# Performance work log

Hardware: AMD Instinct MI355X
Metric: run time of the kernel (lower is better)

The kernel has to match this reference:

```python
import jax, jax.numpy as jnp
import numpy as np

NUM_HEAD = 8
HEAD_DIM = 64
MAX_LEN = 2048
FEAT_DIM = 512
BATCH = 2
TEMPERATURE = 10000.0


def positional_encoding(L, F, temperature=TEMPERATURE):
    # Faithful port of get_positional_encoding (torch.range is inclusive -> L / F elements)
    embed = jnp.arange(L, dtype=jnp.float32)
    dim_t = jnp.arange(F, dtype=jnp.float32)
    dim_t = temperature ** (2.0 * jnp.floor(dim_t / 2.0) / F)
    pos = embed[:, None] / dim_t                      # (L, F)
    pos = jnp.stack([jnp.sin(pos[:, 0::2]), jnp.cos(pos[:, 1::2])], axis=2)  # (L, F//2, 2)
    return pos.reshape(1, L, F)


def setup_inputs() -> dict:
    key = jax.random.key(0)
    ks = jax.random.split(key, 7)
    D = NUM_HEAD * HEAD_DIM
    scale = 1.0 / np.sqrt(FEAT_DIM)
    return {
        "inputs": jax.random.normal(ks[0], (BATCH, FEAT_DIM, MAX_LEN), dtype=jnp.float32),
        "Wq": jax.random.normal(ks[1], (D, FEAT_DIM), dtype=jnp.float32) * scale,
        "bq": jax.random.normal(ks[2], (D,), dtype=jnp.float32) * 0.01,
        "Wk": jax.random.normal(ks[3], (D, FEAT_DIM), dtype=jnp.float32) * scale,
        "bk": jax.random.normal(ks[4], (D,), dtype=jnp.float32) * 0.01,
        "Wv": jax.random.normal(ks[5], (D, FEAT_DIM), dtype=jnp.float32) * scale,
        "bv": jax.random.normal(ks[6], (D,), dtype=jnp.float32) * 0.01,
    }


def reference(inputs, Wq, bq, Wk, bk, Wv, bv):
    B, F, L = inputs.shape
    H, d = NUM_HEAD, HEAD_DIM
    pos = positional_encoding(L, F)                   # (1, L, F)
    x = jnp.transpose(inputs, (0, 2, 1))              # (B, L, F)
    qk_in = x + pos
    q = (qk_in @ Wq.T + bq).reshape(B, L, H, d)       # (B, L, H, d)
    k = (qk_in @ Wk.T + bk).reshape(B, L, H, d)
    v = x @ Wv.T + bv                                 # computed but unused (bug in original)
    del v
    # NOTE: original uses KEY heads as values (multi_head_value built from key)
    scores = jnp.einsum("bqhd,bkhd->bhqk", q, k) * (float(d) ** -0.5)
    attn = jax.nn.softmax(scores, axis=-1)            # (B, H, L, L)
    dist = jnp.einsum("bhqk,bkhd->bqhd", attn, k).reshape(B, L, H * d)
    attn_out = jnp.transpose(attn, (0, 2, 3, 1))      # (B, L, L, H) == cat of head splits on -1
    return dist, attn_out
```

## Files before the change

kernel.cpp:

```cpp
#include <hip/hip_runtime.h>
#include <math.h>

constexpr int LSEQ = 2048;
constexpr int FEAT = 512;
constexpr int NH = 8;
constexpr int DM = 512;
constexpr int NB = 2;

typedef __bf16 bf16x8 __attribute__((ext_vector_type(8)));
typedef unsigned short u16x8 __attribute__((ext_vector_type(8)));
typedef unsigned int u32x4 __attribute__((ext_vector_type(4)));
typedef float f32x4 __attribute__((ext_vector_type(4)));

__device__ inline f32x4 mfma16(u16x8 a, u16x8 b, f32x4 c) {
  return __builtin_amdgcn_mfma_f32_16x16x32_bf16(
      __builtin_bit_cast(bf16x8, a), __builtin_bit_cast(bf16x8, b), c, 0, 0, 0);
}
__device__ inline unsigned cvtpk(float lo, float hi) {
  unsigned r;
  asm("v_cvt_pk_bf16_f32 %0, %1, %2" : "=v"(r) : "v"(lo), "v"(hi));
  return r;
}
__device__ inline u16x8 ldbf8(const unsigned short* p) {
  return *reinterpret_cast<const u16x8*>(p);
}

__global__ __launch_bounds__(256) void pos_kernel(float* __restrict__ posT) {
  int idx = blockIdx.x * 256 + threadIdx.x;
  int l = idx & (LSEQ - 1);
  int f = idx >> 11;
  int i = f >> 1;
  double t = exp((double)i * (9.210340371976184 / 256.0));
  float ang = (float)((double)l / t);
  posT[idx] = (f & 1) ? cosf(ang) : sinf(ang);
}

__global__ __launch_bounds__(256) void prep_kernel(const float* __restrict__ x,
                                                   const float* __restrict__ posT,
                                                   unsigned short* __restrict__ abuf) {
  __shared__ float As[64 * 68];
  const int t = threadIdx.x;
  const int bid = blockIdx.x;
  const int ft = bid & 7, lt = (bid >> 3) & 31, b = bid >> 8;
  const int f0 = ft * 64, l0 = lt * 64;
#pragma unroll
  for (int rep = 0; rep < 4; ++rep) {
    int fl = rep * 16 + (t >> 4), l4 = (t & 15) * 4;
    float4 xv = *(const float4*)(x + ((size_t)b * FEAT + f0 + fl) * LSEQ + l0 + l4);
    float4 pv = *(const float4*)(posT + (size_t)(f0 + fl) * LSEQ + l0 + l4);
    *(float4*)&As[fl * 68 + l4] = make_float4(xv.x + pv.x, xv.y + pv.y, xv.z + pv.z, xv.w + pv.w);
  }
  __syncthreads();
  const int ll = t >> 2, fc = t & 3;
#pragma unroll
  for (int rep = 0; rep < 4; ++rep) {
    int fb = (fc + rep * 4) * 4;
    float v0 = As[(fb + 0) * 68 + ll];
    float v1 = As[(fb + 1) * 68 + ll];
    float v2 = As[(fb + 2) * 68 + ll];
    float v3 = As[(fb + 3) * 68 + ll];
    uint2 u = make_uint2(cvtpk(v0, v1), cvtpk(v2, v3));
    *(uint2*)(abuf + ((size_t)(b * LSEQ + l0 + ll)) * 512 + f0 + fb) = u;
  }
}

__global__ __launch_bounds__(256) void wcvt_kernel(const float* __restrict__ Wq,
                                                   const float* __restrict__ Wk,
                                                   unsigned short* __restrict__ wbuf) {
  int i8 = blockIdx.x * 256 + threadIdx.x;
  size_t base = (size_t)i8 * 8;
  const float* src = (base < (size_t)512 * 512) ? Wq + base : Wk + (base - (size_t)512 * 512);
  float4 a = *(const float4*)src;
  float4 b4 = *(const float4*)(src + 4);
  *(uint2*)(wbuf + base) = make_uint2(cvtpk(a.x, a.y), cvtpk(a.z, a.w));
  *(uint2*)(wbuf + base + 4) = make_uint2(cvtpk(b4.x, b4.y), cvtpk(b4.z, b4.w));
}

__global__ __launch_bounds__(256) void proj_kernel(
    const unsigned short* __restrict__ abuf, const unsigned short* __restrict__ wbuf,
    const float* __restrict__ bq, const float* __restrict__ bk,
    unsigned short* __restrict__ qb, unsigned short* __restrict__ kb,
    unsigned short* __restrict__ kT) {
  const int t = threadIdx.x;
  const int c0 = blockIdx.x * 64;
  const int r0 = blockIdx.y * 64;
  const int w = t >> 6, l = t & 63;
  const int lr = l & 15, g = l >> 4;
  const int c0w = c0 + (w >> 1) * 32;
  const int r0w = r0 + (w & 1) * 32;
  f32x4 acc[2][2];
#pragma unroll
  for (int i = 0; i < 2; ++i)
#pragma unroll
    for (int j = 0; j < 2; ++j) acc[i][j] = (f32x4){0.f, 0.f, 0.f, 0.f};
  for (int f0 = 0; f0 < FEAT; f0 += 32) {
    u16x8 a0 = ldbf8(wbuf + (size_t)(c0w + lr) * 512 + f0 + g * 8);
    u16x8 a1 = ldbf8(wbuf + (size_t)(c0w + 16 + lr) * 512 + f0 + g * 8);
    u16x8 b0 = ldbf8(abuf + (size_t)(r0w + lr) * 512 + f0 + g * 8);
    u16x8 b1 = ldbf8(abuf + (size_t)(r0w + 16 + lr) * 512 + f0 + g * 8);
    acc[0][0] = mfma16(a0, b0, acc[0][0]);
    acc[0][1] = mfma16(a0, b1, acc[0][1]);
    acc[1][0] = mfma16(a1, b0, acc[1][0]);
    acc[1][1] = mfma16(a1, b1, acc[1][1]);
  }
  const int isK = (c0 >= DM);
  const float* bias = isK ? bk : bq;
  unsigned short* ob = isK ? kb : qb;
  const int cb = c0w & (DM - 1);
#pragma unroll
  for (int ch = 0; ch < 2; ++ch) {
    int c = cb + ch * 16 + g * 4;
    float b0v = bias[c], b1v = bias[c + 1], b2v = bias[c + 2], b3v = bias[c + 3];
#pragma unroll
    for (int rh = 0; rh < 2; ++rh) {
      int r = r0w + rh * 16 + lr;
      f32x4 v = acc[ch][rh];
      uint2 u = make_uint2(cvtpk(v[0] + b0v, v[1] + b1v), cvtpk(v[2] + b2v, v[3] + b3v));
      *(uint2*)(ob + (size_t)r * 512 + c) = u;
      if (isK) {
        int bsel = r >> 11, lq = r & (LSEQ - 1);
        unsigned short* kp = kT + ((size_t)(bsel * 512 + c)) * 2048 + lq;
        kp[0] = (unsigned short)(u.x & 0xffff);
        kp[2048] = (unsigned short)(u.x >> 16);
        kp[2 * 2048] = (unsigned short)(u.y & 0xffff);
        kp[3 * 2048] = (unsigned short)(u.y >> 16);
      }
    }
  }
}

__global__ __launch_bounds__(512) void pass1_kernel(
    const unsigned short* __restrict__ qb, const unsigned short* __restrict__ kb,
    float* __restrict__ lpart) {
  const int t = threadIdx.x;
  const int bid = blockIdx.x;
  const int sp = bid & 3, qt = (bid >> 2) & 63, b = bid >> 8;
  const int q0 = qt * 32;
  const int h = t >> 6, l = t & 63;
  const int lr = l & 15, g = l >> 4;
  u16x8 qf[2][2];
#pragma unroll
  for (int Mt = 0; Mt < 2; ++Mt)
#pragma unroll
    for (int dh = 0; dh < 2; ++dh)
      qf[Mt][dh] = ldbf8(qb + (size_t)(b * LSEQ + q0 + Mt * 16 + lr) * 512 + h * 64 + dh * 32 + g * 8);
  float sum[2] = {0.f, 0.f};
  for (int slab = 0; slab < 16; ++slab) {
    const int kk0 = sp * 512 + slab * 32;
    u16x8 af[2][2];
#pragma unroll
    for (int kh = 0; kh < 2; ++kh)
#pragma unroll
      for (int dh = 0; dh < 2; ++dh)
        af[kh][dh] = ldbf8(kb + (size_t)(b * LSEQ + kk0 + kh * 16 + lr) * 512 + h * 64 + dh * 32 + g * 8);
#pragma unroll
    for (int Mt = 0; Mt < 2; ++Mt)
#pragma unroll
      for (int kh = 0; kh < 2; ++kh) {
        f32x4 s = (f32x4){0.f, 0.f, 0.f, 0.f};
        s = mfma16(af[kh][0], qf[Mt][0], s);
        s = mfma16(af[kh][1], qf[Mt][1], s);
        sum[Mt] += __expf(s[0] * 0.125f) + __expf(s[1] * 0.125f) +
                   __expf(s[2] * 0.125f) + __expf(s[3] * 0.125f);
      }
  }
#pragma unroll
  for (int Mt = 0; Mt < 2; ++Mt) {
    float v = sum[Mt];
    v += __shfl_xor(v, 16);
    v += __shfl_xor(v, 32);
    if ((l & 48) == 0)
      lpart[((size_t)((b * 4 + sp) * LSEQ) + q0 + Mt * 16 + lr) * 8 + h] = v;
  }
}

__global__ __launch_bounds__(512) void pass2_kernel(
    const unsigned short* __restrict__ qb, const unsigned short* __restrict__ kb,
    const unsigned short* __restrict__ kT, const float* __restrict__ lpart,
    float* __restrict__ attn, float* __restrict__ distp, int log2S) {
  __shared__ float Ps[32 * 292];
  __shared__ float linv[256];
  const int t = threadIdx.x;
  const int bid = blockIdx.x;
  const int S = 1 << log2S;
  const int sp = bid & (S - 1);
  const int qt = (bid >> log2S) & 63;
  const int b = bid >> (6 + log2S);
  const int q0 = qt * 32;
  if (t < 256) {
    int q = t >> 3, hh = t & 7;
    float s = 0.f;
#pragma unroll
    for (int p = 0; p < 4; ++p)
      s += lpart[((size_t)((b * 4 + p) * LSEQ) + q0 + q) * 8 + hh];
    linv[t] = 1.0f / s;
  }
  __syncthreads();
  const int h = t >> 6, l = t & 63;
  const int lr = l & 15, g = l >> 4;
  u16x8 qf[2][2];
#pragma unroll
  for (int Mt = 0; Mt < 2; ++Mt)
#pragma unroll
    for (int dh = 0; dh < 2; ++dh)
      qf[Mt][dh] = ldbf8(qb + (size_t)(b * LSEQ + q0 + Mt * 16 + lr) * 512 + h * 64 + dh * 32 + g * 8);
  float lv[2] = {linv[lr * 8 + h], linv[(16 + lr) * 8 + h]};
  f32x4 dacc[2][4];
#pragma unroll
  for (int Mt = 0; Mt < 2; ++Mt)
#pragma unroll
    for (int Nd = 0; Nd < 4; ++Nd) dacc[Mt][Nd] = (f32x4){0.f, 0.f, 0.f, 0.f};

  const int nslab = 64 >> log2S;
  const int kkb = sp * (2048 >> log2S);
  for (int slab = 0; slab < nslab; ++slab) {
    const int kk0 = kkb + slab * 32;
    u16x8 af[2][2];
#pragma unroll
    for (int kh = 0; kh < 2; ++kh)
#pragma unroll
      for (int dh = 0; dh < 2; ++dh)
        af[kh][dh] = ldbf8(kb + (size_t)(b * LSEQ + kk0 + kh * 16 + lr) * 512 + h * 64 + dh * 32 + g * 8);
    u16x8 bt[4];
#pragma unroll
    for (int Nd = 0; Nd < 4; ++Nd)
      bt[Nd] = ldbf8(kT + (size_t)(b * 512 + h * 64 + Nd * 16 + lr) * 2048 + kk0 + g * 8);
#pragma unroll
    for (int Mt = 0; Mt < 2; ++Mt)
#pragma unroll
      for (int kh = 0; kh < 2; ++kh) {
        f32x4 s = (f32x4){0.f, 0.f, 0.f, 0.f};
        s = mfma16(af[kh][0], qf[Mt][0], s);
        s = mfma16(af[kh][1], qf[Mt][1], s);
        float e0 = __expf(s[0] * 0.125f) * lv[Mt];
        float e1 = __expf(s[1] * 0.125f) * lv[Mt];
        float e2 = __expf(s[2] * 0.125f) * lv[Mt];
        float e3 = __expf(s[3] * 0.125f) * lv[Mt];
        int base = (Mt * 16 + lr) * 292 + h * 36 + kh * 16 + g * 4;
        *(float2*)&Ps[base] = make_float2(e0, e1);
        *(float2*)&Ps[base + 2] = make_float2(e2, e3);
      }
    __syncthreads();
#pragma unroll
    for (int rep = 0; rep < 4; ++rep) {
      int F = rep * 512 + t;
      int q = F >> 6, kk = (F >> 1) & 31, hh = (F & 1) * 4;
      int pb = q * 292 + hh * 36 + kk;
      float4 v = make_float4(Ps[pb], Ps[pb + 36], Ps[pb + 72], Ps[pb + 108]);
      *(float4*)(attn + ((size_t)(b * LSEQ + q0 + q)) * (LSEQ * NH) + (size_t)(kk0 + kk) * 8 + hh) = v;
    }
#pragma unroll
    for (int Mt = 0; Mt < 2; ++Mt) {
      int pb = (Mt * 16 + lr) * 292 + h * 36 + g * 8;
      f32x4 plo = *(const f32x4*)&Ps[pb];
      f32x4 phi = *(const f32x4*)&Ps[pb + 4];
      u32x4 pu = {cvtpk(plo[0], plo[1]), cvtpk(plo[2], plo[3]),
                  cvtpk(phi[0], phi[1]), cvtpk(phi[2], phi[3])};
      u16x8 pa = __builtin_bit_cast(u16x8, pu);
#pragma unroll
      for (int Nd = 0; Nd < 4; ++Nd)
        dacc[Mt][Nd] = mfma16(pa, bt[Nd], dacc[Mt][Nd]);
    }
    __syncthreads();
  }
  float* dp = distp + (size_t)sp * (NB * LSEQ * DM);
#pragma unroll
  for (int Mt = 0; Mt < 2; ++Mt)
#pragma unroll
    for (int Nd = 0; Nd < 4; ++Nd)
#pragma unroll
      for (int r = 0; r < 4; ++r)
        dp[((size_t)(b * LSEQ + q0 + Mt * 16 + g * 4 + r)) * 512 + h * 64 + Nd * 16 + lr] =
            dacc[Mt][Nd][r];
}

__global__ __launch_bounds__(256) void combine_kernel(const float* __restrict__ p,
                                                      float* __restrict__ dist) {
  int i4 = blockIdx.x * 256 + threadIdx.x;
  const int N4 = (NB * LSEQ * DM) / 4;
  const float4* p4 = (const float4*)p;
  float4 a = p4[i4], c = p4[N4 + i4];
  ((float4*)dist)[i4] = make_float4(a.x + c.x, a.y + c.y, a.z + c.z, a.w + c.w);
}

extern "C" void kernel_launch(void* const* d_in, const int* in_sizes, int n_in,
                              void* d_out, int out_size, void* d_ws, size_t ws_size,
                              hipStream_t stream) {
  const float* x  = (const float*)d_in[0];
  const float* Wq = (const float*)d_in[1];
  const float* bq = (const float*)d_in[2];
  const float* Wk = (const float*)d_in[3];
  const float* bk = (const float*)d_in[4];
  float* out  = (float*)d_out;
  float* dist = out;
  float* attn = out + (size_t)NB * LSEQ * DM;
  float* ws = (float*)d_ws;
  float* posT  = ws;
  float* lpart = ws + 1048576;
  unsigned short* abuf = (unsigned short*)(ws + 1179648);
  unsigned short* wbuf = (unsigned short*)(ws + 2228224);
  unsigned short* qb   = (unsigned short*)(ws + 2490368);
  unsigned short* kb   = (unsigned short*)(ws + 3538944);
  unsigned short* kT   = (unsigned short*)(ws + 4587520);
  float* distp = ws + 5636096;
  const int log2S = (ws_size >= (size_t)(5636096 + 2ull * 2097152) * 4) ? 1 : 0;

  pos_kernel<<<4096, 256, 0, stream>>>(posT);
  prep_kernel<<<512, 256, 0, stream>>>(x, posT, abuf);
  wcvt_kernel<<<256, 256, 0, stream>>>(Wq, Wk, wbuf);
  proj_kernel<<<dim3(16, 64), 256, 0, stream>>>(abuf, wbuf, bq, bk, qb, kb, kT);
  pass1_kernel<<<512, 512, 0, stream>>>(qb, kb, lpart);
  float* dtarget = (log2S == 0) ? dist : distp;
  pass2_kernel<<<NB * 64 * (1 << log2S), 512, 0, stream>>>(qb, kb, kT, lpart, attn, dtarget, log2S);
  if (log2S)
    combine_kernel<<<2048, 256, 0, stream>>>(distp, dist);
}
```

Baseline: 178.9 us.

## Split pass2 into four key partitions, use exp2, nontemporal attn stores

Allows pass2 to split the key range four ways when the workspace is large enough, raising the block count to fill more CUs, and generalizes the combine kernel to sum S partials. Replaces __expf of the scaled score with exp2f and a pre-multiplied log2e constant. Writes the large attention output with nontemporal stores to avoid cache pollution, and adds a min-blocks hint to launch bounds. In exchange, the extra split costs more partial-sum memory traffic in combine, and the occupancy hint may force register spills.

```diff
diff --git a/kernel.cpp b/kernel.cpp
--- a/kernel.cpp
+++ b/kernel.cpp
@@ -11,6 +11,8 @@
 typedef unsigned short u16x8 __attribute__((ext_vector_type(8)));
 typedef unsigned int u32x4 __attribute__((ext_vector_type(4)));
 typedef float f32x4 __attribute__((ext_vector_type(4)));
+
+#define EXPC 0.18033688011112042f
 
 __device__ inline f32x4 mfma16(u16x8 a, u16x8 b, f32x4 c) {
   return __builtin_amdgcn_mfma_f32_16x16x32_bf16(
@@ -129,7 +131,7 @@
   }
 }
 
-__global__ __launch_bounds__(512) void pass1_kernel(
+__global__ __launch_bounds__(512, 4) void pass1_kernel(
     const unsigned short* __restrict__ qb, const unsigned short* __restrict__ kb,
     float* __restrict__ lpart) {
   const int t = threadIdx.x;
@@ -160,8 +162,8 @@
         f32x4 s = (f32x4){0.f, 0.f, 0.f, 0.f};
         s = mfma16(af[kh][0], qf[Mt][0], s);
         s = mfma16(af[kh][1], qf[Mt][1], s);
-        sum[Mt] += __expf(s[0] * 0.125f) + __expf(s[1] * 0.125f) +
-                   __expf(s[2] * 0.125f) + __expf(s[3] * 0.125f);
+        sum[Mt] += exp2f(s[0] * EXPC) + exp2f(s[1] * EXPC) +
+                   exp2f(s[2] * EXPC) + exp2f(s[3] * EXPC);
       }
   }
 #pragma unroll
@@ -174,7 +176,7 @@
   }
 }
 
-__global__ __launch_bounds__(512) void pass2_kernel(
+__global__ __launch_bounds__(512, 4) void pass2_kernel(
     const unsigned short* __restrict__ qb, const unsigned short* __restrict__ kb,
     const unsigned short* __restrict__ kT, const float* __restrict__ lpart,
     float* __restrict__ attn, float* __restrict__ distp, int log2S) {
@@ -232,10 +234,10 @@
         f32x4 s = (f32x4){0.f, 0.f, 0.f, 0.f};
         s = mfma16(af[kh][0], qf[Mt][0], s);
         s = mfma16(af[kh][1], qf[Mt][1], s);
-        float e0 = __expf(s[0] * 0.125f) * lv[Mt];
-        float e1 = __expf(s[1] * 0.125f) * lv[Mt];
-        float e2 = __expf(s[2] * 0.125f) * lv[Mt];
-        float e3 = __expf(s[3] * 0.125f) * lv[Mt];
+        float e0 = exp2f(s[0] * EXPC) * lv[Mt];
+        float e1 = exp2f(s[1] * EXPC) * lv[Mt];
+        float e2 = exp2f(s[2] * EXPC) * lv[Mt];
+        float e3 = exp2f(s[3] * EXPC) * lv[Mt];
         int base = (Mt * 16 + lr) * 292 + h * 36 + kh * 16 + g * 4;
         *(float2*)&Ps[base] = make_float2(e0, e1);
         *(float2*)&Ps[base + 2] = make_float2(e2, e3);
@@ -246,8 +248,9 @@
       int F = rep * 512 + t;
       int q = F >> 6, kk = (F >> 1) & 31, hh = (F & 1) * 4;
       int pb = q * 292 + hh * 36 + kk;
-      float4 v = make_float4(Ps[pb], Ps[pb + 36], Ps[pb + 72], Ps[pb + 108]);
-      *(float4*)(attn + ((size_t)(b * LSEQ + q0 + q)) * (LSEQ * NH) + (size_t)(kk0 + kk) * 8 + hh) = v;
+      f32x4 v = {Ps[pb], Ps[pb + 36], Ps[pb + 72], Ps[pb + 108]};
+      __builtin_nontemporal_store(v,
+          (f32x4*)(attn + ((size_t)(b * LSEQ + q0 + q)) * (LSEQ * NH) + (size_t)(kk0 + kk) * 8 + hh));
     }
 #pragma unroll
     for (int Mt = 0; Mt < 2; ++Mt) {
@@ -275,12 +278,16 @@
 }
 
 __global__ __launch_bounds__(256) void combine_kernel(const float* __restrict__ p,
-                                                      float* __restrict__ dist) {
+                                                      float* __restrict__ dist, int S) {
   int i4 = blockIdx.x * 256 + threadIdx.x;
   const int N4 = (NB * LSEQ * DM) / 4;
   const float4* p4 = (const float4*)p;
-  float4 a = p4[i4], c = p4[N4 + i4];
-  ((float4*)dist)[i4] = make_float4(a.x + c.x, a.y + c.y, a.z + c.z, a.w + c.w);
+  float4 s = p4[i4];
+  for (int sp = 1; sp < S; ++sp) {
+    float4 v = p4[(size_t)sp * N4 + i4];
+    s.x += v.x; s.y += v.y; s.z += v.z; s.w += v.w;
+  }
+  ((float4*)dist)[i4] = s;
 }
 
 extern "C" void kernel_launch(void* const* d_in, const int* in_sizes, int n_in,
@@ -303,7 +310,10 @@
   unsigned short* kb   = (unsigned short*)(ws + 3538944);
   unsigned short* kT   = (unsigned short*)(ws + 4587520);
   float* distp = ws + 5636096;
-  const int log2S = (ws_size >= (size_t)(5636096 + 2ull * 2097152) * 4) ? 1 : 0;
+  int log2S;
+  if (ws_size >= (size_t)(5636096 + 4ull * 2097152) * 4) log2S = 2;
+  else if (ws_size >= (size_t)(5636096 + 2ull * 2097152) * 4) log2S = 1;
+  else log2S = 0;
 
   pos_kernel<<<4096, 256, 0, stream>>>(posT);
   prep_kernel<<<512, 256, 0, stream>>>(x, posT, abuf);
@@ -313,5 +323,5 @@
   float* dtarget = (log2S == 0) ? dist : distp;
   pass2_kernel<<<NB * 64 * (1 << log2S), 512, 0, stream>>>(qb, kb, kT, lpart, attn, dtarget, log2S);
   if (log2S)
-    combine_kernel<<<2048, 256, 0, stream>>>(distp, dist);
-}
+    combine_kernel<<<2048, 256, 0, stream>>>(distp, dist, 1 << log2S);
+}
```

New measurement: 177.9 us. Within noise of the previous version (-0.6%).
